# Kernel tuning notes

Measured on AMD Instinct MI355X. Metric: run time of the kernel, lower is better.

Reference implementation:

```python
import jax, jax.numpy as jnp
import numpy as np

B, M, D = 16384, 40, 32
INPUT_DIM = M * D  # 1280
CIN_SIZES = [128, 128]
DEEP_DIMS = [256, 128, 64]
EPS = 1e-5


def _init_linear(key, fan_in, fan_out):
    k1, k2 = jax.random.split(key)
    bound = 1.0 / np.sqrt(fan_in)
    w = jax.random.uniform(k1, (fan_out, fan_in), jnp.float32, -bound, bound)
    b = jax.random.uniform(k2, (fan_out,), jnp.float32, -bound, bound)
    return w, b


def setup_inputs() -> dict:
    key = jax.random.key(0)
    ks = jax.random.split(key, 12)
    x = jax.random.normal(ks[0], (B, INPUT_DIM), jnp.float32)
    emb_3d = jax.random.normal(ks[1], (B, M, D), jnp.float32)
    lin_w, lin_b = _init_linear(ks[2], INPUT_DIM, 1)
    # CIN conv1d (kernel_size=1) weights, flattened to [out, in]
    conv_w0, conv_b0 = _init_linear(ks[3], M * M, CIN_SIZES[0])          # in = 40*40
    prev1 = CIN_SIZES[0] // 2                                             # split_half
    conv_w1, conv_b1 = _init_linear(ks[4], M * prev1, CIN_SIZES[1])       # in = 40*64
    cin_out_dim = CIN_SIZES[0] // 2 + CIN_SIZES[1]                        # 192
    cin_out_w, cin_out_b = _init_linear(ks[5], cin_out_dim, 1)
    dims = [INPUT_DIM] + DEEP_DIMS
    deep_w0, deep_b0 = _init_linear(ks[6], dims[0], dims[1])
    deep_w1, deep_b1 = _init_linear(ks[7], dims[1], dims[2])
    deep_w2, deep_b2 = _init_linear(ks[8], dims[2], dims[3])
    ln_g0, ln_b0 = jnp.ones((dims[1],), jnp.float32), jnp.zeros((dims[1],), jnp.float32)
    ln_g1, ln_b1 = jnp.ones((dims[2],), jnp.float32), jnp.zeros((dims[2],), jnp.float32)
    ln_g2, ln_b2 = jnp.ones((dims[3],), jnp.float32), jnp.zeros((dims[3],), jnp.float32)
    return dict(x=x, emb_3d=emb_3d, lin_w=lin_w, lin_b=lin_b,
                conv_w0=conv_w0, conv_b0=conv_b0, conv_w1=conv_w1, conv_b1=conv_b1,
                cin_out_w=cin_out_w, cin_out_b=cin_out_b,
                deep_w0=deep_w0, deep_b0=deep_b0, ln_g0=ln_g0, ln_b0=ln_b0,
                deep_w1=deep_w1, deep_b1=deep_b1, ln_g1=ln_g1, ln_b1=ln_b1,
                deep_w2=deep_w2, deep_b2=deep_b2, ln_g2=ln_g2, ln_b2=ln_b2)


def _layernorm(h, g, b):
    mu = jnp.mean(h, axis=-1, keepdims=True)
    var = jnp.mean(jnp.square(h - mu), axis=-1, keepdims=True)
    return (h - mu) * jax.lax.rsqrt(var + EPS) * g + b


def _cin_layer(x0, xi, w, b):
    # outer = einsum('bmd,bnd->bmnd') then 1x1 conv over flattened (m*n).
    # Fused: contract the (m,n) outer product directly with the conv weight.
    o = w.shape[0]
    m, n = x0.shape[1], xi.shape[1]
    w3 = w.reshape(o, m, n)
    out = jnp.einsum('bmd,bnd,omn->bod', x0, xi, w3) + b[None, :, None]
    return jax.nn.relu(out)


def reference(x, emb_3d, lin_w, lin_b,
              conv_w0, conv_b0, conv_w1, conv_b1, cin_out_w, cin_out_b,
              deep_w0, deep_b0, ln_g0, ln_b0,
              deep_w1, deep_b1, ln_g1, ln_b1,
              deep_w2, deep_b2, ln_g2, ln_b2):
    aux = (x @ lin_w.T + lin_b)[:, 0]  # [B]

    # CIN with split_half=True
    x0 = emb_3d                                   # [B, 40, 32]
    out0 = _cin_layer(x0, x0, conv_w0, conv_b0)    # [B, 128, 32]
    h1, direct0 = jnp.split(out0, 2, axis=1)       # hidden gets FIRST half
    out1 = _cin_layer(x0, h1, conv_w1, conv_b1)    # [B, 128, 32]
    cin_feat = jnp.sum(jnp.concatenate([direct0, out1], axis=1), axis=2)  # [B, 192]
    aux = aux + (cin_feat @ cin_out_w.T + cin_out_b)[:, 0]

    # Deep tower (dropout = identity in eval)
    h = jax.nn.relu(_layernorm(x @ deep_w0.T + deep_b0, ln_g0, ln_b0))
    h = jax.nn.relu(_layernorm(h @ deep_w1.T + deep_b1, ln_g1, ln_b1))
    h = jax.nn.relu(_layernorm(h @ deep_w2.T + deep_b2, ln_g2, ln_b2))
    return h, aux
```

## Files before the change

### kernel.cpp

```cpp
#include <hip/hip_runtime.h>
#include <hip/hip_bf16.h>

typedef unsigned int u32;
typedef __attribute__((ext_vector_type(8))) short short8;
typedef __attribute__((ext_vector_type(8))) _Float16 half8;
typedef __attribute__((ext_vector_type(4))) float f32x4;

__device__ __forceinline__ u32 bf16_rne(float f) {
  u32 u = __builtin_bit_cast(u32, f);
  return (u + 0x7fffu + ((u >> 16) & 1u)) >> 16;
}
__device__ __forceinline__ u32 pk_bf16(float a, float b) {
  union { __hip_bfloat162 h; u32 u; } cv;
  cv.h = __float22bfloat162_rn(make_float2(a, b));
  return cv.u;
}
__device__ __forceinline__ unsigned short f16b(float f) {
  return __builtin_bit_cast(unsigned short, (_Float16)f);
}
__device__ __forceinline__ half8 splat8(_Float16 x) {
  return (half8){x, x, x, x, x, x, x, x};
}

__device__ __forceinline__ void glds16(const u32* g, u32* l) {
  __builtin_amdgcn_global_load_lds((const __attribute__((address_space(1))) u32*)g,
                                   (__attribute__((address_space(3))) u32*)l, 16, 0, 0);
}

__global__ void swz_kernel(const float* __restrict__ W, unsigned short* __restrict__ out,
                           int N, int K) {
  int tid = blockIdx.x * 256 + threadIdx.x;
  if (tid >= N * K) return;
  int j = tid & 7, l = (tid >> 3) & 63, rest = tid >> 9;
  int nt = N >> 4;
  int t = rest % nt, k32 = rest / nt;
  int o = t * 16 + (l & 15);
  int k = k32 * 32 + (l >> 4) * 8 + j;
  out[tid] = (unsigned short)bf16_rne(W[(size_t)o * K + k]);
}
__global__ void swz_f16_kernel(const float* __restrict__ W, unsigned short* __restrict__ out,
                               int N, int K) {
  int tid = blockIdx.x * 256 + threadIdx.x;
  if (tid >= N * K) return;
  int j = tid & 7, l = (tid >> 3) & 63, rest = tid >> 9;
  int nt = N >> 4;
  int t = rest % nt, k32 = rest / nt;
  int o = t * 16 + (l & 15);
  int k = k32 * 32 + (l >> 4) * 8 + j;
  out[tid] = f16b(W[(size_t)o * K + k]);
}

__global__ void tbl_kernel(u32* __restrict__ tbl0) {
  int g = threadIdx.x;
  if (g >= 120) return;
  int base = 0, m = 0;
  for (m = 0; m < 40; ++m) {
    int cnt = 5 - (m >> 3);
    if (g < base + cnt) break;
    base += cnt;
  }
  int n0 = 8 * ((m >> 3) + (g - base));
  tbl0[g] = (u32)m | ((u32)n0 << 8);
}

__global__ void swz0s_kernel(const float* __restrict__ W, const u32* __restrict__ tbl0,
                             unsigned short* __restrict__ out) {
  int tid = blockIdx.x * 256 + threadIdx.x;
  if (tid >= 960 * 128) return;
  int j = tid & 7, l = (tid >> 3) & 63, rest = tid >> 9;
  int t = rest & 7, k32 = rest >> 3;
  int o = t * 16 + (l & 15);
  int g = k32 * 4 + (l >> 4);
  u32 te = tbl0[g];
  int m = (int)(te & 255u), n0 = (int)(te >> 8);
  int n = n0 + j;
  float val;
  if (n < m) val = 0.f;
  else if (n == m) val = W[o * 1600 + m * 41];
  else val = W[o * 1600 + m * 40 + n] + W[o * 1600 + n * 40 + m];
  out[tid] = f16b(val);
}

__global__ __launch_bounds__(256, 2) void cin_kernel(
    const float* __restrict__ emb, const unsigned short* __restrict__ wz0s,
    const unsigned short* __restrict__ wz1, const u32* __restrict__ tbl0,
    const float* __restrict__ b0v, const float* __restrict__ b1v,
    const float* __restrict__ cw, float* __restrict__ aux) {
  __shared__ __align__(16) unsigned short Xh[128 * 40];
  __shared__ __align__(16) unsigned short h1s[128 * 72];
  __shared__ u32 tbl[120];
  __shared__ float auxacc[128];

  const int tid = threadIdx.x;
  const int lane = tid & 63;
  const int w = tid >> 6;
  const int wr = w >> 1, wc = w & 1;
  const int rl = lane & 15, q = lane >> 4;
  const int b0blk = blockIdx.x * 4;

#pragma unroll
  for (int i = 0; i < 5; ++i) {
    int idx = i * 256 + tid;
    int b = idx / 320;
    int rem = idx - b * 320;
    int m = rem >> 3, d0 = (rem & 7) * 4;
    float4 v = *(const float4*)(emb + ((size_t)(b0blk + b) * 40 + m) * 32 + d0);
    unsigned short* xc = &Xh[(b * 32 + d0) * 40 + m];
    xc[0] = f16b(v.x); xc[40] = f16b(v.y); xc[80] = f16b(v.z); xc[120] = f16b(v.w);
  }
  if (tid < 128) auxacc[tid] = 0.f;
  if (tid < 120) tbl[tid] = tbl0[tid];
  __syncthreads();

  f32x4 acc[4][4];
#pragma unroll
  for (int u = 0; u < 4; ++u)
#pragma unroll
    for (int t = 0; t < 4; ++t) acc[u][t] = f32x4{0.f, 0.f, 0.f, 0.f};

  {
    const u32* bptr = (const u32*)wz0s + wc * 1024 + lane * 4;
    const u32* xw = (const u32*)Xh;
    uint4 bA[4], bB[4];
    uint4 vnA[4], vnB[4];
    _Float16 xmA[4], xmB[4];

    auto loadB0 = [&](int kc, uint4* b) {
#pragma unroll
      for (int tt = 0; tt < 4; ++tt) b[tt] = *(const uint4*)(bptr + kc * 2048 + tt * 256);
    };
    auto loadA0 = [&](int kc, uint4* vn, _Float16* xm) {
      u32 te = tbl[kc * 4 + q];
      int mm = (int)(te & 255u);
      int w0 = (int)(te >> 8) >> 1;
#pragma unroll
      for (int u = 0; u < 4; ++u) {
        int r = 64 * wr + 16 * u + rl;
        vn[u] = *(const uint4*)(xw + r * 20 + w0);
        xm[u] = __builtin_bit_cast(_Float16, Xh[r * 40 + mm]);
      }
    };
    auto mfma0 = [&](const uint4* vn, const _Float16* xm, const uint4* bv) {
      __builtin_amdgcn_s_setprio(1);
#pragma unroll
      for (int u = 0; u < 4; ++u) {
        half8 af = __builtin_bit_cast(half8, vn[u]) * splat8(xm[u]);
#pragma unroll
        for (int tt = 0; tt < 4; ++tt)
          acc[u][tt] = __builtin_amdgcn_mfma_f32_16x16x32_f16(
              af, __builtin_bit_cast(half8, bv[tt]), acc[u][tt], 0, 0, 0);
      }
      __builtin_amdgcn_s_setprio(0);
    };

    loadB0(0, bA);
    loadA0(0, vnA, xmA);
    for (int kc = 0; kc < 30; kc += 2) {
      loadB0(kc + 1, bB);
      loadA0(kc + 1, vnB, xmB);
      mfma0(vnA, xmA, bA);
      int kn = (kc + 2 < 30) ? kc + 2 : 0;
      loadB0(kn, bA);
      loadA0(kn, vnA, xmA);
      mfma0(vnB, xmB, bB);
    }
  }

  if (wc == 0) {
#pragma unroll
    for (int u = 0; u < 4; ++u) {
      int r0q = 64 * wr + 16 * u + 4 * q;
#pragma unroll
      for (int tt = 0; tt < 4; ++tt) {
        int o = 16 * tt + rl;
        float bb = b0v[o];
#pragma unroll
        for (int i = 0; i < 4; ++i) {
          float vv = fmaxf(acc[u][tt][i] + bb, 0.f);
          h1s[(r0q + i) * 72 + o] = f16b(vv);
        }
      }
    }
  } else {
#pragma unroll
    for (int u = 0; u < 4; ++u)
#pragma unroll
      for (int i = 0; i < 4; ++i) {
        float sle = 0.f;
#pragma unroll
        for (int tt = 0; tt < 4; ++tt) {
          int o = 64 + 16 * tt + rl;
          sle += fmaxf(acc[u][tt][i] + b0v[o], 0.f) * cw[o - 64];
        }
        sle += __shfl_xor(sle, 1, 16);
        sle += __shfl_xor(sle, 2, 16);
        sle += __shfl_xor(sle, 4, 16);
        sle += __shfl_xor(sle, 8, 16);
        if (rl == 0) atomicAdd(&auxacc[64 * wr + 16 * u + 4 * q + i], sle);
      }
  }
#pragma unroll
  for (int u = 0; u < 4; ++u)
#pragma unroll
    for (int t = 0; t < 4; ++t) acc[u][t] = f32x4{0.f, 0.f, 0.f, 0.f};
  __syncthreads();

  {
    const u32* bptr = (const u32*)wz1 + wc * 1024 + lane * 4;
    const u32* hw = (const u32*)h1s;
    uint4 bA[4], bB[4];
    uint4 hpA[4], hpB[4];
    _Float16 xmA[4], xmB[4];

    auto loadB1 = [&](int kc, uint4* b) {
#pragma unroll
      for (int tt = 0; tt < 4; ++tt) b[tt] = *(const uint4*)(bptr + kc * 2048 + tt * 256);
    };
    auto loadH = [&](int kc, uint4* hp) {
      int wof = ((kc & 1) << 4) + 4 * q;
#pragma unroll
      for (int u = 0; u < 4; ++u) {
        int r = 64 * wr + 16 * u + rl;
        hp[u] = *(const uint4*)(hw + r * 36 + wof);
      }
    };
    auto loadXM = [&](int kp, _Float16* xm) {
#pragma unroll
      for (int u = 0; u < 4; ++u)
        xm[u] = __builtin_bit_cast(_Float16, Xh[(64 * wr + 16 * u + rl) * 40 + kp]);
    };
    auto mfma1 = [&](const uint4* hp, const _Float16* xm, const uint4* bv) {
      __builtin_amdgcn_s_setprio(1);
#pragma unroll
      for (int u = 0; u < 4; ++u) {
        half8 af = __builtin_bit_cast(half8, hp[u]) * splat8(xm[u]);
#pragma unroll
        for (int tt = 0; tt < 4; ++tt)
          acc[u][tt] = __builtin_amdgcn_mfma_f32_16x16x32_f16(
              af, __builtin_bit_cast(half8, bv[tt]), acc[u][tt], 0, 0, 0);
      }
      __builtin_amdgcn_s_setprio(0);
    };

    loadB1(0, bA);
    loadH(0, hpA);
    loadXM(0, xmA);
    for (int kp = 0; kp < 40; ++kp) {
      int kc = 2 * kp;
      loadB1(kc + 1, bB);
      loadH(kc + 1, hpB);
      mfma1(hpA, xmA, bA);
      int kc2 = (kc + 2 < 80) ? kc + 2 : 0;
      int kn = (kp + 1 < 40) ? kp + 1 : 0;
      loadB1(kc2, bA);
      loadH(kc2, hpA);
      loadXM(kn, xmB);
      mfma1(hpB, xmA, bB);
#pragma unroll
      for (int u = 0; u < 4; ++u) xmA[u] = xmB[u];
    }
  }

#pragma unroll
  for (int u = 0; u < 4; ++u)
#pragma unroll
    for (int i = 0; i < 4; ++i) {
      float sle = 0.f;
#pragma unroll
      for (int tt = 0; tt < 4; ++tt) {
        int o = 64 * wc + 16 * tt + rl;
        sle += fmaxf(acc[u][tt][i] + b1v[o], 0.f) * cw[64 + o];
      }
      sle += __shfl_xor(sle, 1, 16);
      sle += __shfl_xor(sle, 2, 16);
      sle += __shfl_xor(sle, 4, 16);
      sle += __shfl_xor(sle, 8, 16);
      if (rl == 0) atomicAdd(&auxacc[64 * wr + 16 * u + 4 * q + i], sle);
    }
  __syncthreads();
  if (tid < 4) {
    float ssum = 0.f;
    for (int d = 0; d < 32; ++d) ssum += auxacc[tid * 32 + d];
    aux[b0blk + tid] = ssum;
  }
}

template <int NT, bool LAST>
__device__ __forceinline__ void ln_epilogue(
    int tid, int w, int rl, int q, f32x4 (&acc)[2][4],
    const float* __restrict__ bias, const float* __restrict__ g,
    const float* __restrict__ be, float* rs1, float* rs2,
    unsigned short* hout, int hstr, float* __restrict__ Cout, int r0) {
  constexpr int WT = NT / 4;
  constexpr float rN = 1.0f / (float)(NT * 16);
  __syncthreads();
  if (tid < 32) { rs1[tid] = 0.f; rs2[tid] = 0.f; }
  __syncthreads();
  float vals[2][WT][4];
#pragma unroll
  for (int u = 0; u < 2; ++u)
#pragma unroll
    for (int tt = 0; tt < WT; ++tt) {
      int o = (WT * w + tt) * 16 + rl;
      float bb = bias[o];
#pragma unroll
      for (int i = 0; i < 4; ++i) vals[u][tt][i] = acc[u][tt][i] + bb;
    }
#pragma unroll
  for (int u = 0; u < 2; ++u)
#pragma unroll
    for (int i = 0; i < 4; ++i) {
      float s1 = 0.f, s2 = 0.f;
#pragma unroll
      for (int tt = 0; tt < WT; ++tt) {
        float v = vals[u][tt][i];
        s1 += v;
        s2 += v * v;
      }
#pragma unroll
      for (int m = 1; m < 16; m <<= 1) {
        s1 += __shfl_xor(s1, m, 64);
        s2 += __shfl_xor(s2, m, 64);
      }
      if (rl == 0) {
        atomicAdd(&rs1[16 * u + 4 * q + i], s1);
        atomicAdd(&rs2[16 * u + 4 * q + i], s2);
      }
    }
  __syncthreads();
#pragma unroll
  for (int u = 0; u < 2; ++u)
#pragma unroll
    for (int i = 0; i < 4; ++i) {
      int row = 16 * u + 4 * q + i;
      float mu = rs1[row] * rN;
      float rsd = rsqrtf(rs2[row] * rN - mu * mu + 1e-5f);
#pragma unroll
      for (int tt = 0; tt < WT; ++tt) {
        int o = (WT * w + tt) * 16 + rl;
        float y = fmaxf((vals[u][tt][i] - mu) * rsd * g[o] + be[o], 0.f);
        if constexpr (LAST)
          Cout[(size_t)(r0 + row) * (NT * 16) + o] = y;
        else
          hout[row * hstr + o] = (unsigned short)bf16_rne(y);
      }
    }
}

__global__ __launch_bounds__(256, 2) void tower_kernel(
    const float* __restrict__ x, const unsigned short* __restrict__ wzd0,
    const unsigned short* __restrict__ wzd1, const unsigned short* __restrict__ wzd2,
    const float* __restrict__ db0, const float* __restrict__ g0, const float* __restrict__ be0,
    const float* __restrict__ db1, const float* __restrict__ g1, const float* __restrict__ be1,
    const float* __restrict__ db2, const float* __restrict__ g2, const float* __restrict__ be2,
    const float* __restrict__ lw, const float* __restrict__ lb,
    const float* __restrict__ cb, float* __restrict__ aux, float* __restrict__ hout) {
  __shared__ __align__(16) u32 Bt[4096];
  __shared__ __align__(16) unsigned short At[32 * 40];
  __shared__ __align__(16) unsigned short h0[32 * 264];
  __shared__ __align__(16) unsigned short h1[32 * 136];
  __shared__ float rs1[32], rs2[32];

  const int tid = threadIdx.x, lane = tid & 63, w = tid >> 6;
  const int rl = lane & 15, q = lane >> 4;
  const int r0 = blockIdx.x * 32;

  f32x4 acc[2][4];
#pragma unroll
  for (int u = 0; u < 2; ++u)
#pragma unroll
    for (int t = 0; t < 4; ++t) acc[u][t] = f32x4{0.f, 0.f, 0.f, 0.f};
  float lacc = 0.f;

  for (int kk = 0; kk < 1280; kk += 32) {
    __syncthreads();
    {
      int r = tid >> 3, kh = (tid & 7) * 4;
      const float* src = x + (size_t)(r0 + r) * 1280 + kk + kh;
      float4 v0 = *(const float4*)src;
      const float* lwp = lw + kk + kh;
      lacc += v0.x * lwp[0] + v0.y * lwp[1] + v0.z * lwp[2] + v0.w * lwp[3];
      uint2 p;
      p.x = pk_bf16(v0.x, v0.y);
      p.y = pk_bf16(v0.z, v0.w);
      *(uint2*)&At[r * 40 + kh] = p;
      const u32* gb = (const u32*)wzd0 + (size_t)(kk >> 5) * 4096;
#pragma unroll
      for (int j = 0; j < 4; ++j)
        glds16(gb + w * 1024 + j * 256 + lane * 4, &Bt[w * 1024 + j * 256]);
    }
    __syncthreads();
    short8 af[2];
#pragma unroll
    for (int u = 0; u < 2; ++u)
      af[u] = __builtin_bit_cast(short8, *(const uint4*)&At[(16 * u + rl) * 40 + q * 8]);
#pragma unroll
    for (int tt = 0; tt < 4; ++tt) {
      short8 bfv = __builtin_bit_cast(short8, *(const uint4*)&Bt[((4 * w + tt) * 64 + lane) * 4]);
#pragma unroll
      for (int u = 0; u < 2; ++u)
        acc[u][tt] = __builtin_amdgcn_mfma_f32_16x16x32_bf16(af[u], bfv, acc[u][tt], 0, 0, 0);
    }
  }
  lacc += __shfl_xor(lacc, 1, 64);
  lacc += __shfl_xor(lacc, 2, 64);
  lacc += __shfl_xor(lacc, 4, 64);
  if ((tid & 7) == 0) aux[r0 + (tid >> 3)] += lacc + lb[0] + cb[0];

  ln_epilogue<16, false>(tid, w, rl, q, acc, db0, g0, be0, rs1, rs2, h0, 264, nullptr, r0);

#pragma unroll
  for (int u = 0; u < 2; ++u)
#pragma unroll
    for (int t = 0; t < 4; ++t) acc[u][t] = f32x4{0.f, 0.f, 0.f, 0.f};
  for (int kk = 0; kk < 256; kk += 32) {
    __syncthreads();
    {
      const u32* gb = (const u32*)wzd1 + (size_t)(kk >> 5) * 2048;
#pragma unroll
      for (int j = 0; j < 2; ++j)
        glds16(gb + w * 512 + j * 256 + lane * 4, &Bt[w * 512 + j * 256]);
    }
    __syncthreads();
    short8 af[2];
#pragma unroll
    for (int u = 0; u < 2; ++u)
      af[u] = __builtin_bit_cast(short8, *(const uint4*)&h0[(16 * u + rl) * 264 + kk + q * 8]);
#pragma unroll
    for (int tt = 0; tt < 2; ++tt) {
      short8 bfv = __builtin_bit_cast(short8, *(const uint4*)&Bt[((2 * w + tt) * 64 + lane) * 4]);
#pragma unroll
      for (int u = 0; u < 2; ++u)
        acc[u][tt] = __builtin_amdgcn_mfma_f32_16x16x32_bf16(af[u], bfv, acc[u][tt], 0, 0, 0);
    }
  }
  ln_epilogue<8, false>(tid, w, rl, q, acc, db1, g1, be1, rs1, rs2, h1, 136, nullptr, r0);

#pragma unroll
  for (int u = 0; u < 2; ++u)
#pragma unroll
    for (int t = 0; t < 4; ++t) acc[u][t] = f32x4{0.f, 0.f, 0.f, 0.f};
  for (int kk = 0; kk < 128; kk += 32) {
    __syncthreads();
    {
      const u32* gb = (const u32*)wzd2 + (size_t)(kk >> 5) * 1024;
      glds16(gb + w * 256 + lane * 4, &Bt[w * 256]);
    }
    __syncthreads();
    short8 af[2];
#pragma unroll
    for (int u = 0; u < 2; ++u)
      af[u] = __builtin_bit_cast(short8, *(const uint4*)&h1[(16 * u + rl) * 136 + kk + q * 8]);
    short8 bfv = __builtin_bit_cast(short8, *(const uint4*)&Bt[(w * 64 + lane) * 4]);
#pragma unroll
    for (int u = 0; u < 2; ++u)
      acc[u][0] = __builtin_amdgcn_mfma_f32_16x16x32_bf16(af[u], bfv, acc[u][0], 0, 0, 0);
  }
  ln_epilogue<4, true>(tid, w, rl, q, acc, db2, g2, be2, rs1, rs2, nullptr, 0, hout, r0);
}

extern "C" void kernel_launch(void* const* d_in, const int* in_sizes, int n_in,
                              void* d_out, int out_size, void* d_ws, size_t ws_size,
                              hipStream_t stream) {
  const float* x = (const float*)d_in[0];
  const float* emb = (const float*)d_in[1];
  const float* lin_w = (const float*)d_in[2];
  const float* lin_b = (const float*)d_in[3];
  const float* cw0 = (const float*)d_in[4];
  const float* cb0 = (const float*)d_in[5];
  const float* cw1 = (const float*)d_in[6];
  const float* cb1 = (const float*)d_in[7];
  const float* cow = (const float*)d_in[8];
  const float* cob = (const float*)d_in[9];
  const float* dw0 = (const float*)d_in[10];
  const float* db0 = (const float*)d_in[11];
  const float* g0 = (const float*)d_in[12];
  const float* be0 = (const float*)d_in[13];
  const float* dw1 = (const float*)d_in[14];
  const float* db1 = (const float*)d_in[15];
  const float* g1 = (const float*)d_in[16];
  const float* be1 = (const float*)d_in[17];
  const float* dw2 = (const float*)d_in[18];
  const float* db2 = (const float*)d_in[19];
  const float* g2 = (const float*)d_in[20];
  const float* be2 = (const float*)d_in[21];

  char* ws = (char*)d_ws;
  unsigned short* wz0s = (unsigned short*)(ws + 0);
  u32* tbl0 = (u32*)(ws + 245760);
  unsigned short* wz1 = (unsigned short*)(ws + 246272);
  unsigned short* wzd0 = (unsigned short*)(ws + 901632);
  unsigned short* wzd1 = (unsigned short*)(ws + 1556992);
  unsigned short* wzd2 = (unsigned short*)(ws + 1622528);

  float* h_out = (float*)d_out;
  float* aux = h_out + (size_t)16384 * 64;

  tbl_kernel<<<1, 128, 0, stream>>>(tbl0);
  swz0s_kernel<<<480, 256, 0, stream>>>(cw0, tbl0, wz0s);
  swz_f16_kernel<<<(2560 * 128 + 255) / 256, 256, 0, stream>>>(cw1, wz1, 128, 2560);
  swz_kernel<<<(1280 * 256 + 255) / 256, 256, 0, stream>>>(dw0, wzd0, 256, 1280);
  swz_kernel<<<(256 * 128 + 255) / 256, 256, 0, stream>>>(dw1, wzd1, 128, 256);
  swz_kernel<<<(128 * 64 + 255) / 256, 256, 0, stream>>>(dw2, wzd2, 64, 128);

  cin_kernel<<<4096, 256, 0, stream>>>(emb, wz0s, wz1, tbl0, cb0, cb1, cow, aux);

  tower_kernel<<<512, 256, 0, stream>>>(x, wzd0, wzd1, wzd2, db0, g0, be0, db1, g1, be1,
                                        db2, g2, be2, lin_w, lin_b, cob, aux, h_out);
}
```

Measured before the change: 606.2 us.

## Stream tower GEMM operands directly to registers with double-buffered prefetch

Drops the LDS staging buffers and per-k-step barriers in the deep tower kernel. A and B fragments now load straight from global memory into registers with a two-stage ping-pong prefetch, and s_setprio is raised around the MFMA blocks. The cost being attacked is the pair of __syncthreads per k-step and the LDS round trip. In exchange, every wave now loads x redundantly (four waves read the same rows), which raises global/L2 traffic and register pressure. Only wave 0 accumulates the linear term.

Result: no change. 616.7 us (+1.7%).

```diff
diff --git a/kernel.cpp b/kernel.cpp
--- a/kernel.cpp
+++ b/kernel.cpp
@@ -20,11 +20,6 @@
 }
 __device__ __forceinline__ half8 splat8(_Float16 x) {
   return (half8){x, x, x, x, x, x, x, x};
-}
-
-__device__ __forceinline__ void glds16(const u32* g, u32* l) {
-  __builtin_amdgcn_global_load_lds((const __attribute__((address_space(1))) u32*)g,
-                                   (__attribute__((address_space(3))) u32*)l, 16, 0, 0);
 }
 
 __global__ void swz_kernel(const float* __restrict__ W, unsigned short* __restrict__ out,
@@ -355,8 +350,6 @@
     const float* __restrict__ db2, const float* __restrict__ g2, const float* __restrict__ be2,
     const float* __restrict__ lw, const float* __restrict__ lb,
     const float* __restrict__ cb, float* __restrict__ aux, float* __restrict__ hout) {
-  __shared__ __align__(16) u32 Bt[4096];
-  __shared__ __align__(16) unsigned short At[32 * 40];
   __shared__ __align__(16) unsigned short h0[32 * 264];
   __shared__ __align__(16) unsigned short h1[32 * 136];
   __shared__ float rs1[32], rs2[32];
@@ -370,91 +363,141 @@
   for (int u = 0; u < 2; ++u)
 #pragma unroll
     for (int t = 0; t < 4; ++t) acc[u][t] = f32x4{0.f, 0.f, 0.f, 0.f};
-  float lacc = 0.f;
-
-  for (int kk = 0; kk < 1280; kk += 32) {
-    __syncthreads();
-    {
-      int r = tid >> 3, kh = (tid & 7) * 4;
-      const float* src = x + (size_t)(r0 + r) * 1280 + kk + kh;
-      float4 v0 = *(const float4*)src;
-      const float* lwp = lw + kk + kh;
-      lacc += v0.x * lwp[0] + v0.y * lwp[1] + v0.z * lwp[2] + v0.w * lwp[3];
-      uint2 p;
-      p.x = pk_bf16(v0.x, v0.y);
-      p.y = pk_bf16(v0.z, v0.w);
-      *(uint2*)&At[r * 40 + kh] = p;
-      const u32* gb = (const u32*)wzd0 + (size_t)(kk >> 5) * 4096;
-#pragma unroll
-      for (int j = 0; j < 4; ++j)
-        glds16(gb + w * 1024 + j * 256 + lane * 4, &Bt[w * 1024 + j * 256]);
-    }
-    __syncthreads();
-    short8 af[2];
-#pragma unroll
-    for (int u = 0; u < 2; ++u)
-      af[u] = __builtin_bit_cast(short8, *(const uint4*)&At[(16 * u + rl) * 40 + q * 8]);
-#pragma unroll
-    for (int tt = 0; tt < 4; ++tt) {
-      short8 bfv = __builtin_bit_cast(short8, *(const uint4*)&Bt[((4 * w + tt) * 64 + lane) * 4]);
-#pragma unroll
-      for (int u = 0; u < 2; ++u)
-        acc[u][tt] = __builtin_amdgcn_mfma_f32_16x16x32_bf16(af[u], bfv, acc[u][tt], 0, 0, 0);
-    }
-  }
-  lacc += __shfl_xor(lacc, 1, 64);
-  lacc += __shfl_xor(lacc, 2, 64);
-  lacc += __shfl_xor(lacc, 4, 64);
-  if ((tid & 7) == 0) aux[r0 + (tid >> 3)] += lacc + lb[0] + cb[0];
-
+
+  {
+    const float* xr0 = x + (size_t)(r0 + rl) * 1280 + q * 8;
+    const float* xr1 = xr0 + 16 * 1280;
+    const u32* w0p = (const u32*)wzd0 + 4 * w * 256 + lane * 4;
+    float lac0 = 0.f, lac1 = 0.f;
+
+    uint4 bA[4], bB[4];
+    float4 fA[4], fB[4];
+
+    auto loadB = [&](int kc, uint4* b) {
+#pragma unroll
+      for (int tt = 0; tt < 4; ++tt) b[tt] = *(const uint4*)(w0p + kc * 4096 + tt * 256);
+    };
+    auto loadA = [&](int kc, float4* f) {
+      f[0] = *(const float4*)(xr0 + kc * 32);
+      f[1] = *(const float4*)(xr0 + kc * 32 + 4);
+      f[2] = *(const float4*)(xr1 + kc * 32);
+      f[3] = *(const float4*)(xr1 + kc * 32 + 4);
+    };
+    auto dolin = [&](int kc, const float4* f) {
+      if (w == 0) {
+        const float* lp = lw + kc * 32 + q * 8;
+        lac0 += f[0].x * lp[0] + f[0].y * lp[1] + f[0].z * lp[2] + f[0].w * lp[3] +
+                f[1].x * lp[4] + f[1].y * lp[5] + f[1].z * lp[6] + f[1].w * lp[7];
+        lac1 += f[2].x * lp[0] + f[2].y * lp[1] + f[2].z * lp[2] + f[2].w * lp[3] +
+                f[3].x * lp[4] + f[3].y * lp[5] + f[3].z * lp[6] + f[3].w * lp[7];
+      }
+    };
+    auto domfma = [&](const float4* f, const uint4* b) {
+      __builtin_amdgcn_s_setprio(1);
+#pragma unroll
+      for (int u = 0; u < 2; ++u) {
+        uint4 ap;
+        ap.x = pk_bf16(f[2 * u].x, f[2 * u].y);
+        ap.y = pk_bf16(f[2 * u].z, f[2 * u].w);
+        ap.z = pk_bf16(f[2 * u + 1].x, f[2 * u + 1].y);
+        ap.w = pk_bf16(f[2 * u + 1].z, f[2 * u + 1].w);
+        short8 af = __builtin_bit_cast(short8, ap);
+#pragma unroll
+        for (int tt = 0; tt < 4; ++tt)
+          acc[u][tt] = __builtin_amdgcn_mfma_f32_16x16x32_bf16(
+              af, __builtin_bit_cast(short8, b[tt]), acc[u][tt], 0, 0, 0);
+      }
+      __builtin_amdgcn_s_setprio(0);
+    };
+
+    loadB(0, bA);
+    loadA(0, fA);
+    for (int kc = 0; kc < 40; kc += 2) {
+      loadB(kc + 1, bB);
+      loadA(kc + 1, fB);
+      dolin(kc, fA);
+      domfma(fA, bA);
+      int kn = (kc + 2 < 40) ? kc + 2 : 0;
+      loadB(kn, bA);
+      loadA(kn, fA);
+      dolin(kc + 1, fB);
+      domfma(fB, bB);
+    }
+
+    lac0 += __shfl_xor(lac0, 16, 64);
+    lac0 += __shfl_xor(lac0, 32, 64);
+    lac1 += __shfl_xor(lac1, 16, 64);
+    lac1 += __shfl_xor(lac1, 32, 64);
+    if (w == 0 && q == 0) {
+      aux[r0 + rl] += lac0 + lb[0] + cb[0];
+      aux[r0 + 16 + rl] += lac1 + lb[0] + cb[0];
+    }
+  }
   ln_epilogue<16, false>(tid, w, rl, q, acc, db0, g0, be0, rs1, rs2, h0, 264, nullptr, r0);
+  __syncthreads();
 
 #pragma unroll
   for (int u = 0; u < 2; ++u)
 #pragma unroll
     for (int t = 0; t < 4; ++t) acc[u][t] = f32x4{0.f, 0.f, 0.f, 0.f};
-  for (int kk = 0; kk < 256; kk += 32) {
-    __syncthreads();
-    {
-      const u32* gb = (const u32*)wzd1 + (size_t)(kk >> 5) * 2048;
-#pragma unroll
-      for (int j = 0; j < 2; ++j)
-        glds16(gb + w * 512 + j * 256 + lane * 4, &Bt[w * 512 + j * 256]);
-    }
-    __syncthreads();
-    short8 af[2];
-#pragma unroll
-    for (int u = 0; u < 2; ++u)
-      af[u] = __builtin_bit_cast(short8, *(const uint4*)&h0[(16 * u + rl) * 264 + kk + q * 8]);
-#pragma unroll
-    for (int tt = 0; tt < 2; ++tt) {
-      short8 bfv = __builtin_bit_cast(short8, *(const uint4*)&Bt[((2 * w + tt) * 64 + lane) * 4]);
-#pragma unroll
-      for (int u = 0; u < 2; ++u)
-        acc[u][tt] = __builtin_amdgcn_mfma_f32_16x16x32_bf16(af[u], bfv, acc[u][tt], 0, 0, 0);
+  {
+    const u32* w1p = (const u32*)wzd1 + 2 * w * 256 + lane * 4;
+    uint4 bA[2], bB[2];
+    auto loadB = [&](int kc, uint4* b) {
+#pragma unroll
+      for (int tt = 0; tt < 2; ++tt) b[tt] = *(const uint4*)(w1p + kc * 2048 + tt * 256);
+    };
+    auto domfma = [&](int kc, const uint4* b) {
+      __builtin_amdgcn_s_setprio(1);
+#pragma unroll
+      for (int u = 0; u < 2; ++u) {
+        short8 af = __builtin_bit_cast(short8,
+            *(const uint4*)&h0[(16 * u + rl) * 264 + kc * 32 + q * 8]);
+#pragma unroll
+        for (int tt = 0; tt < 2; ++tt)
+          acc[u][tt] = __builtin_amdgcn_mfma_f32_16x16x32_bf16(
+              af, __builtin_bit_cast(short8, b[tt]), acc[u][tt], 0, 0, 0);
+      }
+      __builtin_amdgcn_s_setprio(0);
+    };
+    loadB(0, bA);
+    for (int kc = 0; kc < 8; kc += 2) {
+      loadB(kc + 1, bB);
+      domfma(kc, bA);
+      int kn = (kc + 2 < 8) ? kc + 2 : 0;
+      loadB(kn, bA);
+      domfma(kc + 1, bB);
     }
   }
   ln_epilogue<8, false>(tid, w, rl, q, acc, db1, g1, be1, rs1, rs2, h1, 136, nullptr, r0);
+  __syncthreads();
 
 #pragma unroll
   for (int u = 0; u < 2; ++u)
 #pragma unroll
     for (int t = 0; t < 4; ++t) acc[u][t] = f32x4{0.f, 0.f, 0.f, 0.f};
-  for (int kk = 0; kk < 128; kk += 32) {
-    __syncthreads();
-    {
-      const u32* gb = (const u32*)wzd2 + (size_t)(kk >> 5) * 1024;
-      glds16(gb + w * 256 + lane * 4, &Bt[w * 256]);
-    }
-    __syncthreads();
-    short8 af[2];
-#pragma unroll
-    for (int u = 0; u < 2; ++u)
-      af[u] = __builtin_bit_cast(short8, *(const uint4*)&h1[(16 * u + rl) * 136 + kk + q * 8]);
-    short8 bfv = __builtin_bit_cast(short8, *(const uint4*)&Bt[(w * 64 + lane) * 4]);
-#pragma unroll
-    for (int u = 0; u < 2; ++u)
-      acc[u][0] = __builtin_amdgcn_mfma_f32_16x16x32_bf16(af[u], bfv, acc[u][0], 0, 0, 0);
+  {
+    const u32* w2p = (const u32*)wzd2 + w * 256 + lane * 4;
+    uint4 bA, bB;
+    auto domfma = [&](int kc, uint4 b) {
+      __builtin_amdgcn_s_setprio(1);
+#pragma unroll
+      for (int u = 0; u < 2; ++u) {
+        short8 af = __builtin_bit_cast(short8,
+            *(const uint4*)&h1[(16 * u + rl) * 136 + kc * 32 + q * 8]);
+        acc[u][0] = __builtin_amdgcn_mfma_f32_16x16x32_bf16(
+            af, __builtin_bit_cast(short8, b), acc[u][0], 0, 0, 0);
+      }
+      __builtin_amdgcn_s_setprio(0);
+    };
+    bA = *(const uint4*)(w2p);
+    for (int kc = 0; kc < 4; kc += 2) {
+      bB = *(const uint4*)(w2p + (kc + 1) * 1024);
+      domfma(kc, bA);
+      int kn = (kc + 2 < 4) ? kc + 2 : 0;
+      bA = *(const uint4*)(w2p + kn * 1024);
+      domfma(kc + 1, bB);
+    }
   }
   ln_epilogue<4, true>(tid, w, rl, q, acc, db2, g2, be2, rs1, rs2, nullptr, 0, hout, r0);
 }
```
